# Optimization experiments

Hardware: AMD Instinct MI355X
Metric: run time of the kernel (lower is better)

## Reference

```python
import jax, jax.numpy as jnp
import numpy as np

N_NODES = 100000
N_EDGES = 1600000
D = 64
L = 4
N_GRAPHS = 512
N_TASKS = 1
BN_EPS = 1e-5


def _batchnorm(h, g, b):
    # training-mode BN over node dim, biased variance
    mu = jnp.mean(h, axis=0)
    var = jnp.mean(jnp.square(h - mu), axis=0)
    return g * (h - mu) * jax.lax.rsqrt(var + BN_EPS) + b


def setup_inputs() -> dict:
    key = jax.random.key(0)
    ks = jax.random.split(key, 12)
    s = 1.0 / np.sqrt(D)
    x = jax.random.normal(ks[0], (N_NODES, D), dtype=jnp.float32)
    edge_index = jax.random.randint(ks[1], (2, N_EDGES), 0, N_NODES, dtype=jnp.int32)
    batch = jnp.sort(jax.random.randint(ks[2], (N_NODES,), 0, N_GRAPHS, dtype=jnp.int32))
    return {
        "x": x,
        "edge_index": edge_index,
        "batch": batch,
        "W1": jax.random.uniform(ks[3], (L, D, D), jnp.float32, -s, s),
        "b1": jax.random.uniform(ks[4], (L, D), jnp.float32, -s, s),
        "g1": jnp.ones((L, D), jnp.float32),
        "bt1": jnp.zeros((L, D), jnp.float32),
        "W2": jax.random.uniform(ks[5], (L, D, D), jnp.float32, -s, s),
        "b2": jax.random.uniform(ks[6], (L, D), jnp.float32, -s, s),
        "g2": jnp.ones((L, D), jnp.float32),
        "bt2": jnp.zeros((L, D), jnp.float32),
        "eps": jnp.zeros((L,), jnp.float32),
        "Wh": jax.random.uniform(ks[7], (D, N_TASKS), jnp.float32, -s, s),
        "bh": jax.random.uniform(ks[8], (N_TASKS,), jnp.float32, -s, s),
    }


def reference(x, edge_index, batch, W1, b1, g1, bt1, W2, b2, g2, bt2, eps, Wh, bh):
    src, dst = edge_index[0], edge_index[1]
    h = x
    for i in range(L):
        # GIN aggregation: (1+eps)*x_i + sum_{j->i} x_j (scatter-add over edges)
        agg = jax.ops.segment_sum(h[src], dst, num_segments=N_NODES)
        h = (1.0 + eps[i]) * h + agg
        # MLP: Linear -> BN -> ReLU -> Linear
        h = h @ W1[i] + b1[i]
        h = jax.nn.relu(_batchnorm(h, g1[i], bt1[i]))
        h = h @ W2[i] + b2[i]
        # outer BN + ReLU
        h = jax.nn.relu(_batchnorm(h, g2[i], bt2[i]))
    # global mean pool per graph
    sums = jax.ops.segment_sum(h, batch, num_segments=N_GRAPHS)
    cnt = jax.ops.segment_sum(jnp.ones((N_NODES,), h.dtype), batch, num_segments=N_GRAPHS)
    pooled = sums / jnp.maximum(cnt, 1.0)[:, None]
    return pooled @ Wh + bh
```

## Files before the change

### kernel.cpp

```cpp
#include <hip/hip_runtime.h>

#define BN_EPS 1e-5f

typedef unsigned int  uint_t;
typedef unsigned short ushort_t;
typedef __attribute__((ext_vector_type(8))) short short8;
typedef __attribute__((ext_vector_type(4))) float f32x4;

__device__ __forceinline__ void atomicAdd4(float* p, float4 v) {
    unsafeAtomicAdd(p + 0, v.x);
    unsafeAtomicAdd(p + 1, v.y);
    unsafeAtomicAdd(p + 2, v.z);
    unsafeAtomicAdd(p + 3, v.w);
}

__device__ __forceinline__ float bnr1(float a, float b, float v) {
    return fmaxf(fmaf(a, v, b), 0.0f);
}

__device__ __forceinline__ ushort_t f2bf(float f) {
    uint_t x = __float_as_uint(f);
    uint_t r = x + 0x7fffu + ((x >> 16) & 1u);
    return (ushort_t)(r >> 16);
}
__device__ __forceinline__ uint_t pack2(float a, float b) {
    return ((uint_t)f2bf(b) << 16) | (uint_t)f2bf(a);
}
__device__ __forceinline__ float lo2f(uint_t p) { return __uint_as_float(p << 16); }
__device__ __forceinline__ float hi2f(uint_t p) { return __uint_as_float(p & 0xffff0000u); }
__device__ __forceinline__ float bf2f(ushort_t h) { return __uint_as_float((uint_t)h << 16); }

__global__ __launch_bounds__(256) void k_cast(const float4* __restrict__ X,
        uint2* __restrict__ Xb, int n4)
{
    for (int i = blockIdx.x * 256 + threadIdx.x; i < n4; i += gridDim.x * 256) {
        float4 v = X[i];
        uint2 o;
        o.x = pack2(v.x, v.y);
        o.y = pack2(v.z, v.w);
        Xb[i] = o;
    }
}

__global__ __launch_bounds__(256) void k_wsplit(const float* __restrict__ W1,
        const float* __restrict__ W2, ushort_t* __restrict__ WH,
        ushort_t* __restrict__ WL)
{
    int idx = blockIdx.x * 256 + threadIdx.x;
    int m = idx >> 12;
    int r = idx & 4095;
    int ct = r >> 10;
    int kh = (r >> 9) & 1;
    int l  = (r >> 3) & 63;
    int j  = r & 7;
    int k = kh * 32 + (l >> 4) * 8 + j;
    int c = ct * 16 + (l & 15);
    const float* Wsrc = (m < 4) ? (W1 + (size_t)m * 4096)
                                : (W2 + (size_t)(m - 4) * 4096);
    float w = Wsrc[k * 64 + c];
    ushort_t hb = f2bf(w);
    ushort_t lb = f2bf(w - bf2f(hb));
    WH[idx] = hb;
    WL[idx] = lb;
}

__global__ __launch_bounds__(256) void k_fillell(const int* __restrict__ src,
        const int* __restrict__ dst, int* __restrict__ deg,
        int* __restrict__ ell, int nedges, int M)
{
    int nx = gridDim.x >> 3;
    int x  = blockIdx.x & 7;
    int ci = blockIdx.x >> 3;
    int lo = (int)(((long long)M * x) >> 3);
    int hi = (int)(((long long)M * (x + 1)) >> 3);
    int chunk = (nedges + nx - 1) / nx;
    int e0 = ci * chunk;
    int e1 = min(nedges, e0 + chunk);
    for (int e = e0 + threadIdx.x; e < e1; e += 256) {
        int d = dst[e];
        if (d >= lo && d < hi) {
            int pos = atomicAdd(&deg[d], 1);
            if (pos < 64) ell[(size_t)d * 64 + pos] = src[e];
        }
    }
}

__global__ __launch_bounds__(256) void k_gather(const uint2* __restrict__ H,
        const int* __restrict__ deg, const int* __restrict__ ell,
        const float* __restrict__ Sin, const float* __restrict__ g,
        const float* __restrict__ bt, const float* __restrict__ epsp,
        int layer, uint2* __restrict__ U, int N, float invM)
{
    int lane = threadIdx.x & 63;
    int wv = threadIdx.x >> 6;
    int node = blockIdx.x * 4 + wv;
    if (node >= N) return;
    int q = lane & 15, sub = lane >> 4;

    float4 A4 = make_float4(1.f, 1.f, 1.f, 1.f);
    float4 B4 = make_float4(0.f, 0.f, 0.f, 0.f);
    bool dobn = (Sin != nullptr);
    if (dobn) {
        float as[4], bs[4];
#pragma unroll
        for (int j = 0; j < 4; ++j) {
            int c = q * 4 + j;
            float mu = Sin[c] * invM;
            float var = Sin[64 + c] * invM - mu * mu;
            float a = g[c] * rsqrtf(var + BN_EPS);
            as[j] = a;
            bs[j] = bt[c] - a * mu;
        }
        A4 = make_float4(as[0], as[1], as[2], as[3]);
        B4 = make_float4(bs[0], bs[1], bs[2], bs[3]);
    }

    int n = min(deg[node], 64);
    float4 acc = make_float4(0.f, 0.f, 0.f, 0.f);
    int myidx = (lane < n) ? ell[(size_t)node * 64 + lane] : 0;
    int nIter = (n + 15) >> 4;
    for (int t = 0; t < nIter; ++t) {
        int j0 = t * 16 + sub;
        int j1 = j0 + 4, j2 = j0 + 8, j3 = j0 + 12;
        int s0 = __shfl(myidx, (j0 < n) ? j0 : 0);
        int s1 = __shfl(myidx, (j1 < n) ? j1 : 0);
        int s2 = __shfl(myidx, (j2 < n) ? j2 : 0);
        int s3 = __shfl(myidx, (j3 < n) ? j3 : 0);
        uint2 r0 = H[(size_t)s0 * 16 + q];
        uint2 r1 = H[(size_t)s1 * 16 + q];
        uint2 r2 = H[(size_t)s2 * 16 + q];
        uint2 r3 = H[(size_t)s3 * 16 + q];
        float4 v0 = make_float4(lo2f(r0.x), hi2f(r0.x), lo2f(r0.y), hi2f(r0.y));
        float4 v1 = make_float4(lo2f(r1.x), hi2f(r1.x), lo2f(r1.y), hi2f(r1.y));
        float4 v2 = make_float4(lo2f(r2.x), hi2f(r2.x), lo2f(r2.y), hi2f(r2.y));
        float4 v3 = make_float4(lo2f(r3.x), hi2f(r3.x), lo2f(r3.y), hi2f(r3.y));
        if (dobn) {
            v0.x = bnr1(A4.x, B4.x, v0.x); v0.y = bnr1(A4.y, B4.y, v0.y);
            v0.z = bnr1(A4.z, B4.z, v0.z); v0.w = bnr1(A4.w, B4.w, v0.w);
            v1.x = bnr1(A4.x, B4.x, v1.x); v1.y = bnr1(A4.y, B4.y, v1.y);
            v1.z = bnr1(A4.z, B4.z, v1.z); v1.w = bnr1(A4.w, B4.w, v1.w);
            v2.x = bnr1(A4.x, B4.x, v2.x); v2.y = bnr1(A4.y, B4.y, v2.y);
            v2.z = bnr1(A4.z, B4.z, v2.z); v2.w = bnr1(A4.w, B4.w, v2.w);
            v3.x = bnr1(A4.x, B4.x, v3.x); v3.y = bnr1(A4.y, B4.y, v3.y);
            v3.z = bnr1(A4.z, B4.z, v3.z); v3.w = bnr1(A4.w, B4.w, v3.w);
        }
        if (j0 < n) { acc.x += v0.x; acc.y += v0.y; acc.z += v0.z; acc.w += v0.w; }
        if (j1 < n) { acc.x += v1.x; acc.y += v1.y; acc.z += v1.z; acc.w += v1.w; }
        if (j2 < n) { acc.x += v2.x; acc.y += v2.y; acc.z += v2.z; acc.w += v2.w; }
        if (j3 < n) { acc.x += v3.x; acc.y += v3.y; acc.z += v3.z; acc.w += v3.w; }
    }
    acc.x += __shfl_xor(acc.x, 16); acc.y += __shfl_xor(acc.y, 16);
    acc.z += __shfl_xor(acc.z, 16); acc.w += __shfl_xor(acc.w, 16);
    acc.x += __shfl_xor(acc.x, 32); acc.y += __shfl_xor(acc.y, 32);
    acc.z += __shfl_xor(acc.z, 32); acc.w += __shfl_xor(acc.w, 32);

    if (sub == 0) {
        uint2 hr = H[(size_t)node * 16 + q];
        float4 hv = make_float4(lo2f(hr.x), hi2f(hr.x), lo2f(hr.y), hi2f(hr.y));
        if (dobn) {
            hv.x = bnr1(A4.x, B4.x, hv.x); hv.y = bnr1(A4.y, B4.y, hv.y);
            hv.z = bnr1(A4.z, B4.z, hv.z); hv.w = bnr1(A4.w, B4.w, hv.w);
        }
        float e = 1.0f + epsp[layer];
        float4 o;
        o.x = fmaf(e, hv.x, acc.x); o.y = fmaf(e, hv.y, acc.y);
        o.z = fmaf(e, hv.z, acc.z); o.w = fmaf(e, hv.w, acc.w);
        uint2 ou;
        ou.x = pack2(o.x, o.y);
        ou.y = pack2(o.z, o.w);
        U[(size_t)node * 16 + q] = ou;
    }
}

__global__ __launch_bounds__(256) void k_mgemm(const ushort_t* __restrict__ In,
        const float* __restrict__ Sin, const float* __restrict__ g,
        const float* __restrict__ bt, const ushort_t* __restrict__ Wh_,
        const ushort_t* __restrict__ Wl_, const float* __restrict__ bias,
        ushort_t* __restrict__ Out, float* __restrict__ Sout, int M, int ntiles)
{
    __shared__ float As_[64];
    __shared__ float Bb_[64];
    __shared__ float SRED[4][128];
    int tid = threadIdx.x;
    int l = tid & 63, wv = tid >> 6;
    int lr = l & 15, lg = l >> 4;
    bool dobn = (Sin != nullptr);

    if (tid < 64) {
        if (dobn) {
            float invM = 1.0f / (float)M;
            float mu = Sin[tid] * invM;
            float var = Sin[64 + tid] * invM - mu * mu;
            float a = g[tid] * rsqrtf(var + BN_EPS);
            As_[tid] = a;
            Bb_[tid] = bt[tid] - a * mu;
        } else { As_[tid] = 1.f; Bb_[tid] = 0.f; }
    }
    __syncthreads();

    const short8* WhF = (const short8*)Wh_;
    const short8* WlF = (const short8*)Wl_;
    short8 Bhi[4][2], Blo[4][2];
#pragma unroll
    for (int ct = 0; ct < 4; ++ct) {
#pragma unroll
        for (int kh = 0; kh < 2; ++kh) {
            Bhi[ct][kh] = WhF[(ct * 2 + kh) * 64 + l];
            Blo[ct][kh] = WlF[(ct * 2 + kh) * 64 + l];
        }
    }
    float bsv[4];
#pragma unroll
    for (int ct = 0; ct < 4; ++ct) bsv[ct] = bias[ct * 16 + lr];

    float st_s[4] = {0.f, 0.f, 0.f, 0.f};
    float st_q[4] = {0.f, 0.f, 0.f, 0.f};

    int stride = gridDim.x * 4;
    int t = blockIdx.x * 4 + wv;
    uint4 ua0 = make_uint4(0, 0, 0, 0), ua1 = ua0;
    if (t < ntiles) {
        int ar = min(t * 16 + lr, M - 1);
        const uint4* pa = (const uint4*)(In + (size_t)ar * 64);
        ua0 = pa[lg];
        ua1 = pa[4 + lg];
    }
    while (t < ntiles) {
        int tn = t + stride;
        uint4 un0 = make_uint4(0, 0, 0, 0), un1 = un0;
        if (tn < ntiles) {
            int ar = min(tn * 16 + lr, M - 1);
            const uint4* pa = (const uint4*)(In + (size_t)ar * 64);
            un0 = pa[lg];
            un1 = pa[4 + lg];
        }

        short8 A0, A1;
        if (dobn) {
            float f0[8], f1[8];
            f0[0]=lo2f(ua0.x); f0[1]=hi2f(ua0.x); f0[2]=lo2f(ua0.y); f0[3]=hi2f(ua0.y);
            f0[4]=lo2f(ua0.z); f0[5]=hi2f(ua0.z); f0[6]=lo2f(ua0.w); f0[7]=hi2f(ua0.w);
            f1[0]=lo2f(ua1.x); f1[1]=hi2f(ua1.x); f1[2]=lo2f(ua1.y); f1[3]=hi2f(ua1.y);
            f1[4]=lo2f(ua1.z); f1[5]=hi2f(ua1.z); f1[6]=lo2f(ua1.w); f1[7]=hi2f(ua1.w);
            short8 a0, a1;
#pragma unroll
            for (int j = 0; j < 8; ++j) {
                int k0 = lg * 8 + j;
                int k1 = 32 + lg * 8 + j;
                a0[j] = (short)f2bf(bnr1(As_[k0], Bb_[k0], f0[j]));
                a1[j] = (short)f2bf(bnr1(As_[k1], Bb_[k1], f1[j]));
            }
            A0 = a0; A1 = a1;
        } else {
            union { uint4 u; short8 s; } c0, c1;
            c0.u = ua0; c1.u = ua1;
            A0 = c0.s; A1 = c1.s;
        }

        f32x4 acc[4];
#pragma unroll
        for (int ct = 0; ct < 4; ++ct) {
            f32x4 a; a[0] = bsv[ct]; a[1] = bsv[ct]; a[2] = bsv[ct]; a[3] = bsv[ct];
            acc[ct] = a;
        }
#pragma unroll
        for (int ct = 0; ct < 4; ++ct) {
            acc[ct] = __builtin_amdgcn_mfma_f32_16x16x32_bf16(A0, Bhi[ct][0], acc[ct], 0, 0, 0);
            acc[ct] = __builtin_amdgcn_mfma_f32_16x16x32_bf16(A0, Blo[ct][0], acc[ct], 0, 0, 0);
            acc[ct] = __builtin_amdgcn_mfma_f32_16x16x32_bf16(A1, Bhi[ct][1], acc[ct], 0, 0, 0);
            acc[ct] = __builtin_amdgcn_mfma_f32_16x16x32_bf16(A1, Blo[ct][1], acc[ct], 0, 0, 0);
        }

#pragma unroll
        for (int ct = 0; ct < 4; ++ct) {
#pragma unroll
            for (int r = 0; r < 4; ++r) {
                int row = t * 16 + lg * 4 + r;
                ushort_t pb = f2bf(acc[ct][r]);
                bool ok = row < M;
                if (ok) Out[(size_t)row * 64 + ct * 16 + lr] = pb;
                float rz = ok ? bf2f(pb) : 0.f;
                st_s[ct] += rz;
                st_q[ct] += rz * rz;
            }
        }
        ua0 = un0; ua1 = un1;
        t = tn;
    }

#pragma unroll
    for (int ct = 0; ct < 4; ++ct) {
        st_s[ct] += __shfl_xor(st_s[ct], 16);
        st_q[ct] += __shfl_xor(st_q[ct], 16);
        st_s[ct] += __shfl_xor(st_s[ct], 32);
        st_q[ct] += __shfl_xor(st_q[ct], 32);
    }
    if (l < 16) {
#pragma unroll
        for (int ct = 0; ct < 4; ++ct) {
            SRED[wv][ct * 16 + l] = st_s[ct];
            SRED[wv][64 + ct * 16 + l] = st_q[ct];
        }
    }
    __syncthreads();
    if (tid < 128) {
        float v = SRED[0][tid] + SRED[1][tid] + SRED[2][tid] + SRED[3][tid];
        unsafeAtomicAdd(&Sout[tid], v);
    }
}

__global__ __launch_bounds__(256) void k_pool(const uint2* __restrict__ H,
        const int* __restrict__ batch, const float* __restrict__ Sin,
        const float* __restrict__ g, const float* __restrict__ bt,
        float* __restrict__ POOL, float* __restrict__ CNT,
        int M, int chunk, float invM)
{
    int q = threadIdx.x & 15, rs = threadIdx.x >> 4;
    float as[4], bs[4];
#pragma unroll
    for (int j = 0; j < 4; ++j) {
        int c = q * 4 + j;
        float mu = Sin[c] * invM;
        float var = Sin[64 + c] * invM - mu * mu;
        float a = g[c] * rsqrtf(var + BN_EPS);
        as[j] = a;
        bs[j] = bt[c] - a * mu;
    }
    int start = blockIdx.x * chunk;
    int end = min(M, start + chunk);
    int curg = -1;
    float4 acc = make_float4(0.f, 0.f, 0.f, 0.f);
    float cl = 0.f;
    for (int r = start + rs; r < end; r += 16) {
        int gg = batch[r];
        uint2 hr = H[(size_t)r * 16 + q];
        float4 v = make_float4(lo2f(hr.x), hi2f(hr.x), lo2f(hr.y), hi2f(hr.y));
        v.x = bnr1(as[0], bs[0], v.x); v.y = bnr1(as[1], bs[1], v.y);
        v.z = bnr1(as[2], bs[2], v.z); v.w = bnr1(as[3], bs[3], v.w);
        if (gg != curg) {
            if (curg >= 0) {
                atomicAdd4(POOL + (size_t)curg * 64 + q * 4, acc);
                if (q == 0) unsafeAtomicAdd(CNT + curg, cl);
            }
            curg = gg;
            acc = make_float4(0.f, 0.f, 0.f, 0.f);
            cl = 0.f;
        }
        acc.x += v.x; acc.y += v.y; acc.z += v.z; acc.w += v.w;
        cl += 1.f;
    }
    if (curg >= 0) {
        atomicAdd4(POOL + (size_t)curg * 64 + q * 4, acc);
        if (q == 0) unsafeAtomicAdd(CNT + curg, cl);
    }
}

__global__ __launch_bounds__(256) void k_head(const float* __restrict__ POOL,
        const float* __restrict__ CNT, const float* __restrict__ Wh,
        const float* __restrict__ bh, float* __restrict__ OUT, int ngraph)
{
    int lane = threadIdx.x & 63;
    int wv = threadIdx.x >> 6;
    int gidx = blockIdx.x * 4 + wv;
    if (gidx >= ngraph) return;
    float c = fmaxf(CNT[gidx], 1.0f);
    float v = POOL[(size_t)gidx * 64 + lane] / c * Wh[lane];
#pragma unroll
    for (int off = 1; off < 64; off <<= 1) v += __shfl_xor(v, off);
    if (lane == 0) OUT[gidx] = v + bh[0];
}

extern "C" void kernel_launch(void* const* d_in, const int* in_sizes, int n_in,
                              void* d_out, int out_size, void* d_ws, size_t ws_size,
                              hipStream_t stream)
{
    const float* x   = (const float*)d_in[0];
    const int*   ei  = (const int*)d_in[1];
    const int*   bat = (const int*)d_in[2];
    const float* W1  = (const float*)d_in[3];
    const float* b1  = (const float*)d_in[4];
    const float* g1  = (const float*)d_in[5];
    const float* bt1 = (const float*)d_in[6];
    const float* W2  = (const float*)d_in[7];
    const float* b2  = (const float*)d_in[8];
    const float* g2  = (const float*)d_in[9];
    const float* bt2 = (const float*)d_in[10];
    const float* eps = (const float*)d_in[11];
    const float* Wh  = (const float*)d_in[12];
    const float* bh  = (const float*)d_in[13];
    float* out = (float*)d_out;

    int M = in_sizes[0] / 64;
    int nedges = in_sizes[1] / 2;
    const int* src = ei;
    const int* dst = ei + nedges;
    const int NG = 512;
    float invM = 1.0f / (float)M;
    int ntiles = (M + 15) / 16;

    size_t NE = (size_t)M * 64;
    ushort_t* Xb  = (ushort_t*)d_ws;
    ushort_t* P0b = Xb + NE;
    ushort_t* P1b = P0b + NE;
    ushort_t* Vb  = P1b + NE;
    ushort_t* WH  = Vb + NE;
    ushort_t* WL  = WH + 32768;
    float* S1   = (float*)(WL + 32768);
    float* S2   = S1 + 512;
    float* POOL = S2 + 512;
    float* CNT  = POOL + (size_t)NG * 64;

    int* deg    = (int*)(CNT + NG);
    int* ell    = deg + M;

    hipMemsetAsync(deg, 0, (size_t)M * sizeof(int), stream);
    hipMemsetAsync(S1, 0, (512 + 512 + (size_t)NG * 64 + NG) * sizeof(float), stream);

    k_cast<<<2048, 256, 0, stream>>>((const float4*)x, (uint2*)Xb, M * 16);
    k_wsplit<<<128, 256, 0, stream>>>(W1, W2, WH, WL);

    k_fillell<<<1024, 256, 0, stream>>>(src, dst, deg, ell, nedges, M);

    int gatherGrid = (M + 3) / 4;
    int gemmGrid = (ntiles + 7) / 8;

    const ushort_t* prevZ = Xb;
    for (int i = 0; i < 4; ++i) {
        ushort_t* Ub = (i & 1) ? P1b : P0b;
        const float* Sprev = (i == 0) ? nullptr : (S2 + (size_t)(i - 1) * 128);
        const float* gprev = (i == 0) ? g2 : (g2 + (size_t)(i - 1) * 64);
        const float* bprev = (i == 0) ? bt2 : (bt2 + (size_t)(i - 1) * 64);

        k_gather<<<gatherGrid, 256, 0, stream>>>((const uint2*)prevZ, deg, ell,
                Sprev, gprev, bprev, eps, i, (uint2*)Ub, M, invM);
        k_mgemm<<<gemmGrid, 256, 0, stream>>>(Ub, nullptr, g1, bt1,
                WH + (size_t)i * 4096, WL + (size_t)i * 4096, b1 + i * 64, Vb,
                S1 + (size_t)i * 128, M, ntiles);
        k_mgemm<<<gemmGrid, 256, 0, stream>>>(Vb, S1 + (size_t)i * 128,
                g1 + i * 64, bt1 + i * 64,
                WH + (size_t)(4 + i) * 4096, WL + (size_t)(4 + i) * 4096,
                b2 + i * 64, Ub, S2 + (size_t)i * 128, M, ntiles);
        prevZ = Ub;
    }
    int chunk = (M + 511) / 512;
    k_pool<<<512, 256, 0, stream>>>((const uint2*)prevZ, bat, S2 + 3 * 128,
            g2 + 192, bt2 + 192, POOL, CNT, M, chunk, invM);
    k_head<<<(NG + 3) / 4, 256, 0, stream>>>(POOL, CNT, Wh, bh, out, NG);
}
```

Measured before the change: 525.1 us.

## Gather four nodes per wave, vectorize ELL fill, and retune grids

Each wavefront in the gather kernel now handles four destination nodes and interleaves their neighbour loads, so more memory requests are in flight per wave and the per-node BN setup is amortized. The ELL fill reads edges as int2 pairs and launches twice as many blocks. The GEMM grid is halved, apparently assuming each block covers 16 tiles. The 4-node loop runs to the maximum degree among the four nodes, which can waste work, and it raises register pressure.

```diff
diff --git a/kernel.cpp b/kernel.cpp
--- a/kernel.cpp
+++ b/kernel.cpp
@@ -73,14 +73,27 @@
     int ci = blockIdx.x >> 3;
     int lo = (int)(((long long)M * x) >> 3);
     int hi = (int)(((long long)M * (x + 1)) >> 3);
-    int chunk = (nedges + nx - 1) / nx;
+    int chunk = (((nedges + nx - 1) / nx) + 1) & ~1;
     int e0 = ci * chunk;
     int e1 = min(nedges, e0 + chunk);
-    for (int e = e0 + threadIdx.x; e < e1; e += 256) {
-        int d = dst[e];
-        if (d >= lo && d < hi) {
-            int pos = atomicAdd(&deg[d], 1);
-            if (pos < 64) ell[(size_t)d * 64 + pos] = src[e];
+    for (int e = e0 + threadIdx.x * 2; e < e1; e += 512) {
+        if (e + 1 < e1) {
+            int2 dd = *(const int2*)(dst + e);
+            int2 ss = *(const int2*)(src + e);
+            if (dd.x >= lo && dd.x < hi) {
+                int pos = atomicAdd(&deg[dd.x], 1);
+                if (pos < 64) ell[(size_t)dd.x * 64 + pos] = ss.x;
+            }
+            if (dd.y >= lo && dd.y < hi) {
+                int pos = atomicAdd(&deg[dd.y], 1);
+                if (pos < 64) ell[(size_t)dd.y * 64 + pos] = ss.y;
+            }
+        } else {
+            int d = dst[e];
+            if (d >= lo && d < hi) {
+                int pos = atomicAdd(&deg[d], 1);
+                if (pos < 64) ell[(size_t)d * 64 + pos] = src[e];
+            }
         }
     }
 }
@@ -93,8 +106,8 @@
 {
     int lane = threadIdx.x & 63;
     int wv = threadIdx.x >> 6;
-    int node = blockIdx.x * 4 + wv;
-    if (node >= N) return;
+    int nb = (blockIdx.x * 4 + wv) * 4;
+    if (nb >= N) return;
     int q = lane & 15, sub = lane >> 4;
 
     float4 A4 = make_float4(1.f, 1.f, 1.f, 1.f);
@@ -115,60 +128,85 @@
         B4 = make_float4(bs[0], bs[1], bs[2], bs[3]);
     }
 
-    int n = min(deg[node], 64);
-    float4 acc = make_float4(0.f, 0.f, 0.f, 0.f);
-    int myidx = (lane < n) ? ell[(size_t)node * 64 + lane] : 0;
-    int nIter = (n + 15) >> 4;
+    int n[4], my[4];
+#pragma unroll
+    for (int i = 0; i < 4; ++i) {
+        int nd = nb + i;
+        bool has = nd < N;
+        n[i] = has ? min(deg[nd], 64) : 0;
+        my[i] = (lane < n[i]) ? ell[(size_t)nd * 64 + lane] : 0;
+    }
+    float4 acc[4];
+#pragma unroll
+    for (int i = 0; i < 4; ++i) acc[i] = make_float4(0.f, 0.f, 0.f, 0.f);
+
+    int nIter = 0;
+#pragma unroll
+    for (int i = 0; i < 4; ++i) nIter = max(nIter, (n[i] + 15) >> 4);
+
     for (int t = 0; t < nIter; ++t) {
         int j0 = t * 16 + sub;
         int j1 = j0 + 4, j2 = j0 + 8, j3 = j0 + 12;
-        int s0 = __shfl(myidx, (j0 < n) ? j0 : 0);
-        int s1 = __shfl(myidx, (j1 < n) ? j1 : 0);
-        int s2 = __shfl(myidx, (j2 < n) ? j2 : 0);
-        int s3 = __shfl(myidx, (j3 < n) ? j3 : 0);
-        uint2 r0 = H[(size_t)s0 * 16 + q];
-        uint2 r1 = H[(size_t)s1 * 16 + q];
-        uint2 r2 = H[(size_t)s2 * 16 + q];
-        uint2 r3 = H[(size_t)s3 * 16 + q];
-        float4 v0 = make_float4(lo2f(r0.x), hi2f(r0.x), lo2f(r0.y), hi2f(r0.y));
-        float4 v1 = make_float4(lo2f(r1.x), hi2f(r1.x), lo2f(r1.y), hi2f(r1.y));
-        float4 v2 = make_float4(lo2f(r2.x), hi2f(r2.x), lo2f(r2.y), hi2f(r2.y));
-        float4 v3 = make_float4(lo2f(r3.x), hi2f(r3.x), lo2f(r3.y), hi2f(r3.y));
-        if (dobn) {
-            v0.x = bnr1(A4.x, B4.x, v0.x); v0.y = bnr1(A4.y, B4.y, v0.y);
-            v0.z = bnr1(A4.z, B4.z, v0.z); v0.w = bnr1(A4.w, B4.w, v0.w);
-            v1.x = bnr1(A4.x, B4.x, v1.x); v1.y = bnr1(A4.y, B4.y, v1.y);
-            v1.z = bnr1(A4.z, B4.z, v1.z); v1.w = bnr1(A4.w, B4.w, v1.w);
-            v2.x = bnr1(A4.x, B4.x, v2.x); v2.y = bnr1(A4.y, B4.y, v2.y);
-            v2.z = bnr1(A4.z, B4.z, v2.z); v2.w = bnr1(A4.w, B4.w, v2.w);
-            v3.x = bnr1(A4.x, B4.x, v3.x); v3.y = bnr1(A4.y, B4.y, v3.y);
-            v3.z = bnr1(A4.z, B4.z, v3.z); v3.w = bnr1(A4.w, B4.w, v3.w);
-        }
-        if (j0 < n) { acc.x += v0.x; acc.y += v0.y; acc.z += v0.z; acc.w += v0.w; }
-        if (j1 < n) { acc.x += v1.x; acc.y += v1.y; acc.z += v1.z; acc.w += v1.w; }
-        if (j2 < n) { acc.x += v2.x; acc.y += v2.y; acc.z += v2.z; acc.w += v2.w; }
-        if (j3 < n) { acc.x += v3.x; acc.y += v3.y; acc.z += v3.z; acc.w += v3.w; }
-    }
-    acc.x += __shfl_xor(acc.x, 16); acc.y += __shfl_xor(acc.y, 16);
-    acc.z += __shfl_xor(acc.z, 16); acc.w += __shfl_xor(acc.w, 16);
-    acc.x += __shfl_xor(acc.x, 32); acc.y += __shfl_xor(acc.y, 32);
-    acc.z += __shfl_xor(acc.z, 32); acc.w += __shfl_xor(acc.w, 32);
+#pragma unroll
+        for (int i = 0; i < 4; ++i) {
+            int ni = n[i];
+            int s0 = __shfl(my[i], (j0 < ni) ? j0 : 0);
+            int s1 = __shfl(my[i], (j1 < ni) ? j1 : 0);
+            int s2 = __shfl(my[i], (j2 < ni) ? j2 : 0);
+            int s3 = __shfl(my[i], (j3 < ni) ? j3 : 0);
+            uint2 r0 = H[(size_t)s0 * 16 + q];
+            uint2 r1 = H[(size_t)s1 * 16 + q];
+            uint2 r2 = H[(size_t)s2 * 16 + q];
+            uint2 r3 = H[(size_t)s3 * 16 + q];
+            float4 v0 = make_float4(lo2f(r0.x), hi2f(r0.x), lo2f(r0.y), hi2f(r0.y));
+            float4 v1 = make_float4(lo2f(r1.x), hi2f(r1.x), lo2f(r1.y), hi2f(r1.y));
+            float4 v2 = make_float4(lo2f(r2.x), hi2f(r2.x), lo2f(r2.y), hi2f(r2.y));
+            float4 v3 = make_float4(lo2f(r3.x), hi2f(r3.x), lo2f(r3.y), hi2f(r3.y));
+            if (dobn) {
+                v0.x = bnr1(A4.x, B4.x, v0.x); v0.y = bnr1(A4.y, B4.y, v0.y);
+                v0.z = bnr1(A4.z, B4.z, v0.z); v0.w = bnr1(A4.w, B4.w, v0.w);
+                v1.x = bnr1(A4.x, B4.x, v1.x); v1.y = bnr1(A4.y, B4.y, v1.y);
+                v1.z = bnr1(A4.z, B4.z, v1.z); v1.w = bnr1(A4.w, B4.w, v1.w);
+                v2.x = bnr1(A4.x, B4.x, v2.x); v2.y = bnr1(A4.y, B4.y, v2.y);
+                v2.z = bnr1(A4.z, B4.z, v2.z); v2.w = bnr1(A4.w, B4.w, v2.w);
+                v3.x = bnr1(A4.x, B4.x, v3.x); v3.y = bnr1(A4.y, B4.y, v3.y);
+                v3.z = bnr1(A4.z, B4.z, v3.z); v3.w = bnr1(A4.w, B4.w, v3.w);
+            }
+            if (j0 < ni) { acc[i].x += v0.x; acc[i].y += v0.y; acc[i].z += v0.z; acc[i].w += v0.w; }
+            if (j1 < ni) { acc[i].x += v1.x; acc[i].y += v1.y; acc[i].z += v1.z; acc[i].w += v1.w; }
+            if (j2 < ni) { acc[i].x += v2.x; acc[i].y += v2.y; acc[i].z += v2.z; acc[i].w += v2.w; }
+            if (j3 < ni) { acc[i].x += v3.x; acc[i].y += v3.y; acc[i].z += v3.z; acc[i].w += v3.w; }
+        }
+    }
+#pragma unroll
+    for (int i = 0; i < 4; ++i) {
+        acc[i].x += __shfl_xor(acc[i].x, 16); acc[i].y += __shfl_xor(acc[i].y, 16);
+        acc[i].z += __shfl_xor(acc[i].z, 16); acc[i].w += __shfl_xor(acc[i].w, 16);
+        acc[i].x += __shfl_xor(acc[i].x, 32); acc[i].y += __shfl_xor(acc[i].y, 32);
+        acc[i].z += __shfl_xor(acc[i].z, 32); acc[i].w += __shfl_xor(acc[i].w, 32);
+    }
 
     if (sub == 0) {
-        uint2 hr = H[(size_t)node * 16 + q];
-        float4 hv = make_float4(lo2f(hr.x), hi2f(hr.x), lo2f(hr.y), hi2f(hr.y));
-        if (dobn) {
-            hv.x = bnr1(A4.x, B4.x, hv.x); hv.y = bnr1(A4.y, B4.y, hv.y);
-            hv.z = bnr1(A4.z, B4.z, hv.z); hv.w = bnr1(A4.w, B4.w, hv.w);
-        }
         float e = 1.0f + epsp[layer];
-        float4 o;
-        o.x = fmaf(e, hv.x, acc.x); o.y = fmaf(e, hv.y, acc.y);
-        o.z = fmaf(e, hv.z, acc.z); o.w = fmaf(e, hv.w, acc.w);
-        uint2 ou;
-        ou.x = pack2(o.x, o.y);
-        ou.y = pack2(o.z, o.w);
-        U[(size_t)node * 16 + q] = ou;
+#pragma unroll
+        for (int i = 0; i < 4; ++i) {
+            int nd = nb + i;
+            if (nd < N) {
+                uint2 hr = H[(size_t)nd * 16 + q];
+                float4 hv = make_float4(lo2f(hr.x), hi2f(hr.x), lo2f(hr.y), hi2f(hr.y));
+                if (dobn) {
+                    hv.x = bnr1(A4.x, B4.x, hv.x); hv.y = bnr1(A4.y, B4.y, hv.y);
+                    hv.z = bnr1(A4.z, B4.z, hv.z); hv.w = bnr1(A4.w, B4.w, hv.w);
+                }
+                float4 o;
+                o.x = fmaf(e, hv.x, acc[i].x); o.y = fmaf(e, hv.y, acc[i].y);
+                o.z = fmaf(e, hv.z, acc[i].z); o.w = fmaf(e, hv.w, acc[i].w);
+                uint2 ou;
+                ou.x = pack2(o.x, o.y);
+                ou.y = pack2(o.z, o.w);
+                U[(size_t)nd * 16 + q] = ou;
+            }
+        }
     }
 }
 
@@ -419,10 +457,10 @@
     k_cast<<<2048, 256, 0, stream>>>((const float4*)x, (uint2*)Xb, M * 16);
     k_wsplit<<<128, 256, 0, stream>>>(W1, W2, WH, WL);
 
-    k_fillell<<<1024, 256, 0, stream>>>(src, dst, deg, ell, nedges, M);
-
-    int gatherGrid = (M + 3) / 4;
-    int gemmGrid = (ntiles + 7) / 8;
+    k_fillell<<<2048, 256, 0, stream>>>(src, dst, deg, ell, nedges, M);
+
+    int gatherGrid = (M + 15) / 16;
+    int gemmGrid = (ntiles + 15) / 16;
 
     const ushort_t* prevZ = Xb;
     for (int i = 0; i < 4; ++i) {
```

New measurement: 518.3 us. Within noise of the previous version (-1.3%).
